# Kernel optimization log

Measured on AMD Instinct MI355X. Metric: run time of the kernel, lower is better.

The kernel has to match this reference:

```python
import jax, jax.numpy as jnp
import numpy as np

NEG_INF = -1e30  # stand-in for float('-inf'); avoids inf-inf NaN edge cases, same softmax result


def setup_inputs() -> dict:
    key = jax.random.key(0)
    k1, k2, k3, k4, k5 = jax.random.split(key, 5)
    B, T, C, H = 16, 2048, 200, 64
    x = jax.random.normal(k1, (B, T, C), dtype=jnp.float32)
    # padding mask over key positions, broadcastable to [B, T, T]
    padding_mask = jax.random.randint(k2, (B, 1, T), 0, 2, dtype=jnp.int32)
    # nn.Linear(n_embd, head_size, bias=False) weights, stored as [C, H] so y = x @ W
    Wk = jax.random.normal(k3, (C, H), dtype=jnp.float32) * (C ** -0.5)
    Wq = jax.random.normal(k4, (C, H), dtype=jnp.float32) * (C ** -0.5)
    Wv = jax.random.normal(k5, (C, H), dtype=jnp.float32) * (C ** -0.5)
    return {"x": x, "padding_mask": padding_mask, "Wk": Wk, "Wq": Wq, "Wv": Wv}


def reference(x, padding_mask, Wk, Wq, Wv):
    # x: [B,T,C]; padding_mask: [B,1,T] (0 = padded key position)
    k = x @ Wk  # [B,T,H]
    q = x @ Wq  # [B,T,H]
    v = x @ Wv  # [B,T,H]
    scale = k.shape[-1] ** -0.5
    wei = jnp.einsum("bqh,bkh->bqk", q, k) * scale  # [B,T,T]
    # mask padded key columns before softmax
    wei = jnp.where(padding_mask == 0, NEG_INF, wei)
    wei = jax.nn.softmax(wei, axis=-1)
    # mask padded query rows (transpose of padding mask) to exact zero after softmax
    mask_t = jnp.swapaxes(padding_mask, -2, -1)  # [B,T,1]
    wei = jnp.where(mask_t == 0, 0.0, wei)
    # dropout is identity in eval mode
    out = jnp.einsum("bqk,bkh->bqh", wei, v)  # [B,T,H]
    return out
```

## Files before the change

kernel.cpp:

```cpp
#include <hip/hip_runtime.h>


typedef __attribute__((ext_vector_type(8))) __bf16 bf16x8;
typedef __attribute__((ext_vector_type(4))) __bf16 bf16x4;
typedef __attribute__((ext_vector_type(4))) float f32x4;

#define T_SEQ 2048
#define C_DIM 200
#define H_DIM 64
#define BT_TOT 32768
#define QKV_ELEMS 2097152
#define PPAD 72
#define OPAD 68
#define WTF_FULL 36864
#define WTF_ELEMS 38400
#define WTF_A_ELEMS 24576
#define LOG2E 1.44269504088896f

__global__ void prep_w(const float* __restrict__ Wk, const float* __restrict__ Wq,
                       const float* __restrict__ Wv, __bf16* __restrict__ WtF) {
    int idx = blockIdx.x * 256 + threadIdx.x;
    if (idx >= WTF_ELEMS) return;
    int w, c, h;
    if (idx < WTF_FULL) {
        int j = idx & 7, lane = (idx >> 3) & 63;
        int chunk = idx >> 9;
        int t = chunk & 3, rest = chunk >> 2;
        w = rest % 3; int ks = rest / 3;
        c = ks * 32 + (lane >> 4) * 8 + j;
        h = t * 16 + (lane & 15);
    } else {
        int i2 = idx - WTF_FULL;
        int j = i2 & 7, l15 = (i2 >> 3) & 15, t = (i2 >> 7) & 3;
        w = i2 >> 9;
        c = 192 + j;
        h = t * 16 + l15;
    }
    const float* W = (w == 0) ? Wq : (w == 1) ? Wk : Wv;
    float val = W[c * H_DIM + h];
    if (w == 0) val *= 0.125f * LOG2E;
    WtF[idx] = (__bf16)val;
}

__global__ __launch_bounds__(256) void qkv_proj(const float* __restrict__ x,
                                                const __bf16* __restrict__ WtF,
                                                __bf16* __restrict__ qb,
                                                __bf16* __restrict__ kb,
                                                __bf16* __restrict__ vT) {
    __shared__ __bf16 Wl[WTF_A_ELEMS];

    const int tid = threadIdx.x;
    const int wave = tid >> 6, lane = tid & 63, l15 = lane & 15, quad = lane >> 4;
    const int m0b = blockIdx.x * 64;
    const int row0 = m0b + wave * 16;

    f32x4 acc[3][4] = {};

    #pragma unroll
    for (int i = 0; i < 12; ++i) {
        const int c = i * 256 + tid;
        *(bf16x8*)(Wl + c * 8) = *(const bf16x8*)(WtF + c * 8);
    }
    __syncthreads();
    #pragma unroll
    for (int ks = 0; ks < 4; ++ks) {
        const float* xr = x + (size_t)(row0 + l15) * C_DIM + ks * 32 + quad * 8;
        const float4 f0 = *(const float4*)xr;
        const float4 f1 = *(const float4*)(xr + 4);
        bf16x8 a;
        a[0]=(__bf16)f0.x; a[1]=(__bf16)f0.y; a[2]=(__bf16)f0.z; a[3]=(__bf16)f0.w;
        a[4]=(__bf16)f1.x; a[5]=(__bf16)f1.y; a[6]=(__bf16)f1.z; a[7]=(__bf16)f1.w;
        #pragma unroll
        for (int w = 0; w < 3; ++w)
            #pragma unroll
            for (int t = 0; t < 4; ++t) {
                const bf16x8 bf = *(const bf16x8*)(Wl + ((ks * 12 + w * 4 + t) << 9) + lane * 8);
                acc[w][t] = __builtin_amdgcn_mfma_f32_16x16x32_bf16(a, bf, acc[w][t], 0, 0, 0);
            }
    }
    __syncthreads();

    #pragma unroll
    for (int i = 0; i < 7; ++i) {
        const int c = i * 256 + tid;
        if (c < 1728)
            *(bf16x8*)(Wl + c * 8) = *(const bf16x8*)(WtF + WTF_A_ELEMS + c * 8);
    }
    __syncthreads();
    #pragma unroll
    for (int ks = 4; ks < 7; ++ks) {
        bf16x8 a;
        if (ks < 6 || quad == 0) {
            const float* xr = x + (size_t)(row0 + l15) * C_DIM + ks * 32 + quad * 8;
            const float4 f0 = *(const float4*)xr;
            const float4 f1 = *(const float4*)(xr + 4);
            a[0]=(__bf16)f0.x; a[1]=(__bf16)f0.y; a[2]=(__bf16)f0.z; a[3]=(__bf16)f0.w;
            a[4]=(__bf16)f1.x; a[5]=(__bf16)f1.y; a[6]=(__bf16)f1.z; a[7]=(__bf16)f1.w;
        } else {
            #pragma unroll
            for (int j = 0; j < 8; ++j) a[j] = (__bf16)0.f;
        }
        #pragma unroll
        for (int w = 0; w < 3; ++w)
            #pragma unroll
            for (int t = 0; t < 4; ++t) {
                const int off = (ks < 6) ? (((ks - 4) * 12 + w * 4 + t) << 9) + lane * 8
                                         : 12288 + ((w * 4 + t) << 7) + l15 * 8;
                const bf16x8 bf = *(const bf16x8*)(Wl + off);
                acc[w][t] = __builtin_amdgcn_mfma_f32_16x16x32_bf16(a, bf, acc[w][t], 0, 0, 0);
            }
    }

    #pragma unroll
    for (int t = 0; t < 4; ++t)
        #pragma unroll
        for (int r = 0; r < 4; ++r) {
            const size_t m = row0 + quad * 4 + r;
            qb[m * H_DIM + t * 16 + l15] = (__bf16)acc[0][t][r];
            kb[m * H_DIM + t * 16 + l15] = (__bf16)acc[1][t][r];
        }
    __syncthreads();
    #pragma unroll
    for (int t = 0; t < 4; ++t)
        #pragma unroll
        for (int r = 0; r < 4; ++r)
            Wl[(t * 16 + l15) * 72 + wave * 16 + quad * 4 + r] = (__bf16)acc[2][t][r];
    __syncthreads();
    const int bb = m0b >> 11, tloc = m0b & 2047;
    #pragma unroll
    for (int i = 0; i < 2; ++i) {
        const int seg = i * 256 + tid;
        const int h = seg >> 3, s8 = seg & 7;
        *(bf16x8*)(vT + ((size_t)bb * H_DIM + h) * T_SEQ + tloc + s8 * 8) =
            *(const bf16x8*)(Wl + h * 72 + s8 * 8);
    }
}

__global__ __launch_bounds__(256, 2) void attn(const __bf16* __restrict__ qb,
                                               const __bf16* __restrict__ kb,
                                               const __bf16* __restrict__ vT,
                                               const int* __restrict__ pm,
                                               float* __restrict__ out) {
    __shared__ __align__(16) char arena[8192 + 36864];
    float* biasS = (float*)arena;

    const int tid = threadIdx.x;
    const int wave = tid >> 6, lane = tid & 63, l15 = lane & 15, quad = lane >> 4;
    const int ks = wave;
    const int b = blockIdx.y;
    const int q0 = blockIdx.x * 64;
    const size_t bT = (size_t)b * T_SEQ;

    for (int i = tid; i < 512; i += 256) {
        const int4 p4 = *(const int4*)(pm + bT + i * 4);
        biasS[i * 4 + 0] = p4.x ? 0.f : -1e30f;
        biasS[i * 4 + 1] = p4.y ? 0.f : -1e30f;
        biasS[i * 4 + 2] = p4.z ? 0.f : -1e30f;
        biasS[i * 4 + 3] = p4.w ? 0.f : -1e30f;
    }
    __syncthreads();

    bf16x8 qa[4][2];
    #pragma unroll
    for (int mt = 0; mt < 4; ++mt)
        #pragma unroll
        for (int s = 0; s < 2; ++s)
            qa[mt][s] = *(const bf16x8*)(qb + (bT + q0 + mt * 16 + l15) * H_DIM + s * 32 + quad * 8);

    __bf16* P = (__bf16*)(arena + 8192) + wave * (64 * PPAD);
    const __bf16* kbase = kb + bT * H_DIM;
    const __bf16* vbase = vT + (size_t)b * H_DIM * T_SEQ;

    f32x4 oacc[4][4] = {};
    float lsum[4] = {0.f, 0.f, 0.f, 0.f};

    bf16x8 kf[8];
    #pragma unroll
    for (int n = 0; n < 4; ++n)
        #pragma unroll
        for (int s = 0; s < 2; ++s)
            kf[n * 2 + s] = *(const bf16x8*)(kbase + (ks * 512 + n * 16 + l15) * H_DIM + s * 32 + quad * 8);

    for (int kt = 0; kt < 8; ++kt) {
        const int key0 = ks * 512 + kt * 64;

        bf16x8 vf[8];
        #pragma unroll
        for (int t = 0; t < 4; ++t)
            #pragma unroll
            for (int s = 0; s < 2; ++s)
                vf[t * 2 + s] = *(const bf16x8*)(vbase + (size_t)(t * 16 + l15) * T_SEQ + key0 + s * 32 + quad * 8);

        #pragma unroll
        for (int n = 0; n < 4; ++n) {
            const f32x4 bias = *(const f32x4*)(biasS + key0 + n * 16 + quad * 4);
            f32x4 s_[4];
            #pragma unroll
            for (int mt = 0; mt < 4; ++mt) s_[mt] = bias;
            #pragma unroll
            for (int s = 0; s < 2; ++s)
                #pragma unroll
                for (int mt = 0; mt < 4; ++mt)
                    s_[mt] = __builtin_amdgcn_mfma_f32_16x16x32_bf16(kf[n * 2 + s], qa[mt][s], s_[mt], 0, 0, 0);
            #pragma unroll
            for (int mt = 0; mt < 4; ++mt) {
                bf16x4 p4;
                #pragma unroll
                for (int r = 0; r < 4; ++r) {
                    const float e = exp2f(s_[mt][r]);
                    lsum[mt] += e;
                    p4[r] = (__bf16)e;
                }
                *(bf16x4*)(P + (mt * 16 + l15) * PPAD + n * 16 + quad * 4) = p4;
            }
        }

        const int keyn = ks * 512 + ((kt < 7) ? kt + 1 : 7) * 64;
        #pragma unroll
        for (int n = 0; n < 4; ++n)
            #pragma unroll
            for (int s = 0; s < 2; ++s)
                kf[n * 2 + s] = *(const bf16x8*)(kbase + (keyn + n * 16 + l15) * H_DIM + s * 32 + quad * 8);

        bf16x8 pa[4][2];
        #pragma unroll
        for (int mt = 0; mt < 4; ++mt)
            #pragma unroll
            for (int s = 0; s < 2; ++s)
                pa[mt][s] = *(const bf16x8*)(P + (mt * 16 + l15) * PPAD + s * 32 + quad * 8);

        #pragma unroll
        for (int t = 0; t < 4; ++t)
            #pragma unroll
            for (int s = 0; s < 2; ++s)
                #pragma unroll
                for (int mt = 0; mt < 4; ++mt)
                    oacc[mt][t] = __builtin_amdgcn_mfma_f32_16x16x32_bf16(pa[mt][s], vf[t * 2 + s], oacc[mt][t], 0, 0, 0);
    }

    #pragma unroll
    for (int mt = 0; mt < 4; ++mt) {
        lsum[mt] += __shfl_xor(lsum[mt], 16, 64);
        lsum[mt] += __shfl_xor(lsum[mt], 32, 64);
    }

    float* Ocomb = (float*)(arena + 8192);
    float* Lcomb = Ocomb + 64 * OPAD;

    __syncthreads();
    if (ks == 1) {
        #pragma unroll
        for (int mt = 0; mt < 4; ++mt) {
            #pragma unroll
            for (int t = 0; t < 4; ++t)
                #pragma unroll
                for (int r = 0; r < 4; ++r)
                    Ocomb[(mt * 16 + quad * 4 + r) * OPAD + t * 16 + l15] = oacc[mt][t][r];
            if (quad == 0) Lcomb[mt * 16 + l15] = lsum[mt];
        }
    }
    __syncthreads();
    if (ks == 2) {
        #pragma unroll
        for (int mt = 0; mt < 4; ++mt) {
            #pragma unroll
            for (int t = 0; t < 4; ++t)
                #pragma unroll
                for (int r = 0; r < 4; ++r)
                    Ocomb[(mt * 16 + quad * 4 + r) * OPAD + t * 16 + l15] += oacc[mt][t][r];
            if (quad == 0) Lcomb[mt * 16 + l15] += lsum[mt];
        }
    }
    __syncthreads();
    if (ks == 3) {
        #pragma unroll
        for (int mt = 0; mt < 4; ++mt) {
            #pragma unroll
            for (int t = 0; t < 4; ++t)
                #pragma unroll
                for (int r = 0; r < 4; ++r)
                    Ocomb[(mt * 16 + quad * 4 + r) * OPAD + t * 16 + l15] += oacc[mt][t][r];
            if (quad == 0) Lcomb[mt * 16 + l15] += lsum[mt];
        }
    }
    __syncthreads();
    if (ks == 0) {
        #pragma unroll
        for (int mt = 0; mt < 4; ++mt) {
            lsum[mt] += Lcomb[mt * 16 + l15];
            #pragma unroll
            for (int t = 0; t < 4; ++t)
                #pragma unroll
                for (int r = 0; r < 4; ++r)
                    oacc[mt][t][r] += Ocomb[(mt * 16 + quad * 4 + r) * OPAD + t * 16 + l15];
            #pragma unroll
            for (int r = 0; r < 4; ++r) {
                const int qpos = q0 + mt * 16 + quad * 4 + r;
                const float lv = __shfl(lsum[mt], quad * 4 + r, 64);
                const bool qvalid = biasS[qpos] == 0.f;
                const float inv = (qvalid && lv > 0.f) ? 1.f / lv : 0.f;
                #pragma unroll
                for (int t = 0; t < 4; ++t)
                    out[(bT + qpos) * H_DIM + t * 16 + l15] = oacc[mt][t][r] * inv;
            }
        }
    }
}

extern "C" void kernel_launch(void* const* d_in, const int* in_sizes, int n_in,
                              void* d_out, int out_size, void* d_ws, size_t ws_size,
                              hipStream_t stream) {
    const float* x  = (const float*)d_in[0];
    const int* pm   = (const int*)d_in[1];
    const float* Wk = (const float*)d_in[2];
    const float* Wq = (const float*)d_in[3];
    const float* Wv = (const float*)d_in[4];
    float* out = (float*)d_out;

    __bf16* qb  = (__bf16*)d_ws;
    __bf16* kb  = qb + QKV_ELEMS;
    __bf16* vT  = kb + QKV_ELEMS;
    __bf16* WtF = vT + QKV_ELEMS;

    prep_w<<<dim3((WTF_ELEMS + 255) / 256), dim3(256), 0, stream>>>(Wk, Wq, Wv, WtF);
    qkv_proj<<<dim3(BT_TOT / 64), dim3(256), 0, stream>>>(x, WtF, qb, kb, vT);
    attn<<<dim3(T_SEQ / 64, 16), dim3(256), 0, stream>>>(qb, kb, vT, pm, out);
}
```

Before: 123.3 us.

## Split attention keys across eight waves with tree reduction and vectorized output

The attention block grows from 256 to 512 threads, so eight waves each handle 256 keys instead of four waves handling 512, which halves the serial key loop per wave. The serial three-step partial-output combine becomes a tree reduction over four LDS buffers. The final normalization and store are spread across all waves with float4 writes. This adds LDS usage and barriers, and the launch bound of 4 blocks of 512 threads may force register limits and spills.

Measured after the change: 282.5 us. 2.29x slower.

```diff
diff --git a/kernel.cpp b/kernel.cpp
--- a/kernel.cpp
+++ b/kernel.cpp
@@ -136,12 +136,12 @@
     }
 }
 
-__global__ __launch_bounds__(256, 2) void attn(const __bf16* __restrict__ qb,
+__global__ __launch_bounds__(512, 4) void attn(const __bf16* __restrict__ qb,
                                                const __bf16* __restrict__ kb,
                                                const __bf16* __restrict__ vT,
                                                const int* __restrict__ pm,
                                                float* __restrict__ out) {
-    __shared__ __align__(16) char arena[8192 + 36864];
+    __shared__ __align__(16) char arena[8192 + 8 * 64 * PPAD * 2];
     float* biasS = (float*)arena;
 
     const int tid = threadIdx.x;
@@ -151,12 +151,12 @@
     const int q0 = blockIdx.x * 64;
     const size_t bT = (size_t)b * T_SEQ;
 
-    for (int i = tid; i < 512; i += 256) {
-        const int4 p4 = *(const int4*)(pm + bT + i * 4);
-        biasS[i * 4 + 0] = p4.x ? 0.f : -1e30f;
-        biasS[i * 4 + 1] = p4.y ? 0.f : -1e30f;
-        biasS[i * 4 + 2] = p4.z ? 0.f : -1e30f;
-        biasS[i * 4 + 3] = p4.w ? 0.f : -1e30f;
+    {
+        const int4 p4 = *(const int4*)(pm + bT + tid * 4);
+        biasS[tid * 4 + 0] = p4.x ? 0.f : -1e30f;
+        biasS[tid * 4 + 1] = p4.y ? 0.f : -1e30f;
+        biasS[tid * 4 + 2] = p4.z ? 0.f : -1e30f;
+        biasS[tid * 4 + 3] = p4.w ? 0.f : -1e30f;
     }
     __syncthreads();
 
@@ -179,10 +179,10 @@
     for (int n = 0; n < 4; ++n)
         #pragma unroll
         for (int s = 0; s < 2; ++s)
-            kf[n * 2 + s] = *(const bf16x8*)(kbase + (ks * 512 + n * 16 + l15) * H_DIM + s * 32 + quad * 8);
-
-    for (int kt = 0; kt < 8; ++kt) {
-        const int key0 = ks * 512 + kt * 64;
+            kf[n * 2 + s] = *(const bf16x8*)(kbase + (ks * 256 + n * 16 + l15) * H_DIM + s * 32 + quad * 8);
+
+    for (int kt = 0; kt < 4; ++kt) {
+        const int key0 = ks * 256 + kt * 64;
 
         bf16x8 vf[8];
         #pragma unroll
@@ -215,7 +215,7 @@
             }
         }
 
-        const int keyn = ks * 512 + ((kt < 7) ? kt + 1 : 7) * 64;
+        const int keyn = ks * 256 + ((kt < 3) ? kt + 1 : 3) * 64;
         #pragma unroll
         for (int n = 0; n < 4; ++n)
             #pragma unroll
@@ -244,65 +244,67 @@
         lsum[mt] += __shfl_xor(lsum[mt], 32, 64);
     }
 
-    float* Ocomb = (float*)(arena + 8192);
-    float* Lcomb = Ocomb + 64 * OPAD;
-
-    __syncthreads();
-    if (ks == 1) {
+    float* cb = (float*)(arena + 8192);
+    float* Lc = cb + 4 * 64 * OPAD;
+
+    __syncthreads();
+    if (ks >= 4) {
+        float* bo = cb + (ks - 4) * (64 * OPAD);
         #pragma unroll
         for (int mt = 0; mt < 4; ++mt) {
             #pragma unroll
             for (int t = 0; t < 4; ++t)
                 #pragma unroll
                 for (int r = 0; r < 4; ++r)
-                    Ocomb[(mt * 16 + quad * 4 + r) * OPAD + t * 16 + l15] = oacc[mt][t][r];
-            if (quad == 0) Lcomb[mt * 16 + l15] = lsum[mt];
-        }
-    }
-    __syncthreads();
-    if (ks == 2) {
+                    bo[(mt * 16 + quad * 4 + r) * OPAD + t * 16 + l15] = oacc[mt][t][r];
+            if (quad == 0) Lc[(ks - 4) * 64 + mt * 16 + l15] = lsum[mt];
+        }
+    }
+    __syncthreads();
+    if (ks < 4) {
+        float* bo = cb + ks * (64 * OPAD);
         #pragma unroll
         for (int mt = 0; mt < 4; ++mt) {
             #pragma unroll
             for (int t = 0; t < 4; ++t)
                 #pragma unroll
                 for (int r = 0; r < 4; ++r)
-                    Ocomb[(mt * 16 + quad * 4 + r) * OPAD + t * 16 + l15] += oacc[mt][t][r];
-            if (quad == 0) Lcomb[mt * 16 + l15] += lsum[mt];
-        }
-    }
-    __syncthreads();
-    if (ks == 3) {
-        #pragma unroll
-        for (int mt = 0; mt < 4; ++mt) {
-            #pragma unroll
-            for (int t = 0; t < 4; ++t)
-                #pragma unroll
-                for (int r = 0; r < 4; ++r)
-                    Ocomb[(mt * 16 + quad * 4 + r) * OPAD + t * 16 + l15] += oacc[mt][t][r];
-            if (quad == 0) Lcomb[mt * 16 + l15] += lsum[mt];
-        }
-    }
-    __syncthreads();
-    if (ks == 0) {
-        #pragma unroll
-        for (int mt = 0; mt < 4; ++mt) {
-            lsum[mt] += Lcomb[mt * 16 + l15];
-            #pragma unroll
-            for (int t = 0; t < 4; ++t)
-                #pragma unroll
-                for (int r = 0; r < 4; ++r)
-                    oacc[mt][t][r] += Ocomb[(mt * 16 + quad * 4 + r) * OPAD + t * 16 + l15];
-            #pragma unroll
-            for (int r = 0; r < 4; ++r) {
-                const int qpos = q0 + mt * 16 + quad * 4 + r;
-                const float lv = __shfl(lsum[mt], quad * 4 + r, 64);
-                const bool qvalid = biasS[qpos] == 0.f;
-                const float inv = (qvalid && lv > 0.f) ? 1.f / lv : 0.f;
-                #pragma unroll
-                for (int t = 0; t < 4; ++t)
-                    out[(bT + qpos) * H_DIM + t * 16 + l15] = oacc[mt][t][r] * inv;
-            }
+                    bo[(mt * 16 + quad * 4 + r) * OPAD + t * 16 + l15] += oacc[mt][t][r];
+            if (quad == 0) Lc[ks * 64 + mt * 16 + l15] += lsum[mt];
+        }
+    }
+    __syncthreads();
+    {
+        const int bsel = ks >> 2;
+        float* dst = cb + bsel * (64 * OPAD);
+        const float* src = cb + (bsel + 2) * (64 * OPAD);
+        const int r0 = (ks & 3) * 16 + (lane >> 2);
+        const int c0 = (lane & 3) * 16;
+        #pragma unroll
+        for (int k = 0; k < 4; ++k) {
+            f32x4* d = (f32x4*)(dst + r0 * OPAD + c0 + k * 4);
+            *d += *(const f32x4*)(src + r0 * OPAD + c0 + k * 4);
+        }
+        if (ks == 0) Lc[lane] += Lc[128 + lane];
+        if (ks == 4) Lc[64 + lane] += Lc[192 + lane];
+    }
+    __syncthreads();
+    {
+        const int rr = lane >> 3;
+        const int cc = lane & 7;
+        const int row = ks * 8 + rr;
+        const int qpos = q0 + row;
+        const float lv = Lc[row] + Lc[64 + row];
+        const bool qvalid = biasS[qpos] == 0.f;
+        const float inv = (qvalid && lv > 0.f) ? 1.f / lv : 0.f;
+        const float* b0 = cb + row * OPAD;
+        const float* b1 = cb + 64 * OPAD + row * OPAD;
+        #pragma unroll
+        for (int k = 0; k < 2; ++k) {
+            const int col = cc * 8 + k * 4;
+            f32x4 o = *(const f32x4*)(b0 + col) + *(const f32x4*)(b1 + col);
+            o *= inv;
+            *(f32x4*)(out + (bT + qpos) * H_DIM + col) = o;
         }
     }
 }
@@ -324,5 +326,5 @@
 
     prep_w<<<dim3((WTF_ELEMS + 255) / 256), dim3(256), 0, stream>>>(Wk, Wq, Wv, WtF);
     qkv_proj<<<dim3(BT_TOT / 64), dim3(256), 0, stream>>>(x, WtF, qb, kb, vT);
-    attn<<<dim3(T_SEQ / 64, 16), dim3(256), 0, stream>>>(qb, kb, vT, pm, out);
+    attn<<<dim3(T_SEQ / 64, 16), dim3(512), 0, stream>>>(qb, kb, vT, pm, out);
 }
```

## Prefetch V fragments one tile ahead and split P staging into halves

Applied to the files above, without the earlier changes.

V fragments for the next key tile are now loaded after the current tile's PV MFMAs, so global V latency overlaps the following QK and softmax work instead of stalling at the top of each iteration. The score computation is split into two halves, and each half of P is read back from LDS right after it is written. This lets LDS reads interleave with the second half's MFMA and exp work. The cost is higher register pressure from keeping vf live across the loop, which could reduce occupancy.

Measured after the change: 125.9 us. +2.1%, slower.

```diff
diff --git a/kernel.cpp b/kernel.cpp
--- a/kernel.cpp
+++ b/kernel.cpp
@@ -175,24 +175,26 @@
     float lsum[4] = {0.f, 0.f, 0.f, 0.f};
 
     bf16x8 kf[8];
+    bf16x8 vf[8];
     #pragma unroll
     for (int n = 0; n < 4; ++n)
         #pragma unroll
         for (int s = 0; s < 2; ++s)
             kf[n * 2 + s] = *(const bf16x8*)(kbase + (ks * 512 + n * 16 + l15) * H_DIM + s * 32 + quad * 8);
+    #pragma unroll
+    for (int t = 0; t < 4; ++t)
+        #pragma unroll
+        for (int s = 0; s < 2; ++s)
+            vf[t * 2 + s] = *(const bf16x8*)(vbase + (size_t)(t * 16 + l15) * T_SEQ + ks * 512 + s * 32 + quad * 8);
 
     for (int kt = 0; kt < 8; ++kt) {
         const int key0 = ks * 512 + kt * 64;
-
-        bf16x8 vf[8];
-        #pragma unroll
-        for (int t = 0; t < 4; ++t)
-            #pragma unroll
-            for (int s = 0; s < 2; ++s)
-                vf[t * 2 + s] = *(const bf16x8*)(vbase + (size_t)(t * 16 + l15) * T_SEQ + key0 + s * 32 + quad * 8);
-
-        #pragma unroll
-        for (int n = 0; n < 4; ++n) {
+        const int keyn = ks * 512 + ((kt < 7) ? kt + 1 : 7) * 64;
+
+        bf16x8 pa[4][2];
+
+        #pragma unroll
+        for (int n = 0; n < 2; ++n) {
             const f32x4 bias = *(const f32x4*)(biasS + key0 + n * 16 + quad * 4);
             f32x4 s_[4];
             #pragma unroll
@@ -214,28 +216,62 @@
                 *(bf16x4*)(P + (mt * 16 + l15) * PPAD + n * 16 + quad * 4) = p4;
             }
         }
-
-        const int keyn = ks * 512 + ((kt < 7) ? kt + 1 : 7) * 64;
+        #pragma unroll
+        for (int mt = 0; mt < 4; ++mt)
+            pa[mt][0] = *(const bf16x8*)(P + (mt * 16 + l15) * PPAD + quad * 8);
+
+        #pragma unroll
+        for (int n = 2; n < 4; ++n) {
+            const f32x4 bias = *(const f32x4*)(biasS + key0 + n * 16 + quad * 4);
+            f32x4 s_[4];
+            #pragma unroll
+            for (int mt = 0; mt < 4; ++mt) s_[mt] = bias;
+            #pragma unroll
+            for (int s = 0; s < 2; ++s)
+                #pragma unroll
+                for (int mt = 0; mt < 4; ++mt)
+                    s_[mt] = __builtin_amdgcn_mfma_f32_16x16x32_bf16(kf[n * 2 + s], qa[mt][s], s_[mt], 0, 0, 0);
+            #pragma unroll
+            for (int mt = 0; mt < 4; ++mt) {
+                bf16x4 p4;
+                #pragma unroll
+                for (int r = 0; r < 4; ++r) {
+                    const float e = exp2f(s_[mt][r]);
+                    lsum[mt] += e;
+                    p4[r] = (__bf16)e;
+                }
+                *(bf16x4*)(P + (mt * 16 + l15) * PPAD + n * 16 + quad * 4) = p4;
+            }
+        }
+        #pragma unroll
+        for (int mt = 0; mt < 4; ++mt)
+            pa[mt][1] = *(const bf16x8*)(P + (mt * 16 + l15) * PPAD + 32 + quad * 8);
+
         #pragma unroll
         for (int n = 0; n < 4; ++n)
             #pragma unroll
             for (int s = 0; s < 2; ++s)
                 kf[n * 2 + s] = *(const bf16x8*)(kbase + (keyn + n * 16 + l15) * H_DIM + s * 32 + quad * 8);
 
-        bf16x8 pa[4][2];
-        #pragma unroll
-        for (int mt = 0; mt < 4; ++mt)
-            #pragma unroll
-            for (int s = 0; s < 2; ++s)
-                pa[mt][s] = *(const bf16x8*)(P + (mt * 16 + l15) * PPAD + s * 32 + quad * 8);
-
         #pragma unroll
         for (int t = 0; t < 4; ++t)
             #pragma unroll
-            for (int s = 0; s < 2; ++s)
-                #pragma unroll
-                for (int mt = 0; mt < 4; ++mt)
-                    oacc[mt][t] = __builtin_amdgcn_mfma_f32_16x16x32_bf16(pa[mt][s], vf[t * 2 + s], oacc[mt][t], 0, 0, 0);
+            for (int mt = 0; mt < 4; ++mt)
+                oacc[mt][t] = __builtin_amdgcn_mfma_f32_16x16x32_bf16(pa[mt][0], vf[t * 2 + 0], oacc[mt][t], 0, 0, 0);
+
+        #pragma unroll
+        for (int t = 0; t < 4; ++t)
+            #pragma unroll
+            for (int mt = 0; mt < 4; ++mt)
+                oacc[mt][t] = __builtin_amdgcn_mfma_f32_16x16x32_bf16(pa[mt][1], vf[t * 2 + 1], oacc[mt][t], 0, 0, 0);
+
+        if (kt < 7) {
+            #pragma unroll
+            for (int t = 0; t < 4; ++t)
+                #pragma unroll
+                for (int s = 0; s < 2; ++s)
+                    vf[t * 2 + s] = *(const bf16x8*)(vbase + (size_t)(t * 16 + l15) * T_SEQ + keyn + s * 32 + quad * 8);
+        }
     }
 
     #pragma unroll
```
